# Optimization experiments

Measured on AMD Instinct MI355X. Metric: run time of the kernel, lower is better.

Reference implementation:

```python
import jax, jax.numpy as jnp
import numpy as np

H = 64
IN = 4
B = 256
T = 2048

def _uniform(key, shape, k):
    return jax.random.uniform(key, shape, jnp.float32, -k, k)

def setup_inputs() -> dict:
    key = jax.random.key(0)
    ks = jax.random.split(key, 12)
    k = 1.0 / np.sqrt(H)
    x = jax.random.normal(ks[0], (B, T, IN), jnp.float32)
    # bidirectional layer 1 (forward + backward directions); biases fused (b_ih + b_hh)
    Wih_f = _uniform(ks[1], (4 * H, IN), k); Whh_f = _uniform(ks[2], (4 * H, H), k); b_f = _uniform(ks[3], (4 * H,), k)
    Wih_b = _uniform(ks[4], (4 * H, IN), k); Whh_b = _uniform(ks[5], (4 * H, H), k); b_b = _uniform(ks[6], (4 * H,), k)
    # unidirectional layer 2, input 2H
    Wih2 = _uniform(ks[7], (4 * H, 2 * H), k); Whh2 = _uniform(ks[8], (4 * H, H), k); b2 = _uniform(ks[9], (4 * H,), k)
    Wfc = _uniform(ks[10], (1, H), k); bfc = _uniform(ks[11], (1,), k)
    return {"x": x, "Wih_f": Wih_f, "Whh_f": Whh_f, "b_f": b_f,
            "Wih_b": Wih_b, "Whh_b": Whh_b, "b_b": b_b,
            "Wih2": Wih2, "Whh2": Whh2, "b2": b2, "Wfc": Wfc, "bfc": bfc}

def _run_lstm(x, Wih, Whh, b, reverse=False):
    # x: [B, T, D] -> outputs [B, T, H], final h [B, H]
    bsz = x.shape[0]
    hdim = Whh.shape[1]
    pre = jnp.einsum('btd,gd->btg', x, Wih) + b  # [B, T, 4H], input contribution precomputed
    pre = jnp.swapaxes(pre, 0, 1)                # [T, B, 4H]
    h0 = jnp.zeros((bsz, hdim), x.dtype)
    c0 = jnp.zeros((bsz, hdim), x.dtype)
    def step(carry, p):
        h, c = carry
        g = p + h @ Whh.T
        i, f, gg, o = jnp.split(g, 4, axis=-1)  # torch gate order: i, f, g, o
        i = jax.nn.sigmoid(i); f = jax.nn.sigmoid(f)
        gg = jnp.tanh(gg); o = jax.nn.sigmoid(o)
        c = f * c + i * gg
        h = o * jnp.tanh(c)
        return (h, c), h
    (hn, _), hs = jax.lax.scan(step, (h0, c0), pre, reverse=reverse)
    return jnp.swapaxes(hs, 0, 1), hn  # [B, T, H], [B, H]

def reference(x, Wih_f, Whh_f, b_f, Wih_b, Whh_b, b_b, Wih2, Whh2, b2, Wfc, bfc):
    out_f, _ = _run_lstm(x, Wih_f, Whh_f, b_f, reverse=False)
    out_b, _ = _run_lstm(x, Wih_b, Whh_b, b_b, reverse=True)
    out1 = jnp.concatenate([out_f, out_b], axis=-1)  # [B, T, 2H]
    _, hn2 = _run_lstm(out1, Wih2, Whh2, b2, reverse=False)  # final hidden [B, H]
    logits = hn2 @ Wfc.T + bfc  # [B, 1]
    return logits
```

## Files before the change

kernel.cpp:

```cpp
#include <hip/hip_runtime.h>

#define HDIM 64
#define BATCH 256
#define TLEN 2048
#define CH 16

typedef float v2f __attribute__((ext_vector_type(2)));

__device__ __forceinline__ float rcp_fast(float x) { return __builtin_amdgcn_rcpf(x); }
__device__ __forceinline__ float sigmoid_fast(float x) { return rcp_fast(1.0f + __expf(-x)); }
__device__ __forceinline__ float tanh_fast(float x)    { return 1.0f - 2.0f * rcp_fast(1.0f + __expf(2.0f * x)); }

__device__ __forceinline__ float dpp_xor1_add(float x) {
    int v = __builtin_amdgcn_update_dpp(0, __float_as_int(x), 0xB1, 0xF, 0xF, true);
    return x + __int_as_float(v);
}
__device__ __forceinline__ float dpp_xor2_add(float x) {
    int v = __builtin_amdgcn_update_dpp(0, __float_as_int(x), 0x4E, 0xF, 0xF, true);
    return x + __int_as_float(v);
}
__device__ __forceinline__ float swz_xor4_add(float x) {
    int v = __builtin_amdgcn_ds_swizzle(__float_as_int(x), 0x101F);
    return x + __int_as_float(v);
}

__device__ __forceinline__ void pk2(v2f& acc, float ax, float ay, float bx, float by) {
    v2f a = {ax, ay}, b = {bx, by};
    acc = __builtin_elementwise_fma(a, b, acc);
}
__device__ __forceinline__ void pk4(v2f& acc, const float4 a, const float4 b) {
    pk2(acc, a.x, a.y, b.x, b.y);
    pk2(acc, a.z, a.w, b.z, b.w);
}

__global__ __launch_bounds__(256, 2)
void lstm_layer1(const float* __restrict__ x,
                 const float* __restrict__ Wih_f, const float* __restrict__ Whh_f, const float* __restrict__ b_f,
                 const float* __restrict__ Wih_b, const float* __restrict__ Whh_b, const float* __restrict__ b_b,
                 float* __restrict__ out1)
{
    const int bidx = blockIdx.x >> 1;
    const int dir  = blockIdx.x & 1;
    const float* __restrict__ Wih = dir ? Wih_b : Wih_f;
    const float* __restrict__ Whh = dir ? Whh_b : Whh_f;
    const float* __restrict__ bb  = dir ? b_b   : b_f;

    const int tid = threadIdx.x;
    const int u   = tid >> 2;
    const int p   = tid & 3;

    __shared__ float xlds[TLEN * 4];
    __shared__ float hbuf[2][HDIM];

    {
        const float4* src = (const float4*)(x + (size_t)bidx * TLEN * 4);
        float4* dst = (float4*)xlds;
        #pragma unroll
        for (int i = 0; i < 8; ++i) dst[tid + 256 * i] = src[tid + 256 * i];
    }
    if (tid < 2 * HDIM) ((float*)hbuf)[tid] = 0.f;

    const float* wbase = Whh + (size_t)u * HDIM + 16 * p;
    const float4 W00 = *(const float4*)(wbase + 0*4096 +  0), W01 = *(const float4*)(wbase + 0*4096 +  4),
                 W02 = *(const float4*)(wbase + 0*4096 +  8), W03 = *(const float4*)(wbase + 0*4096 + 12);
    const float4 W10 = *(const float4*)(wbase + 1*4096 +  0), W11 = *(const float4*)(wbase + 1*4096 +  4),
                 W12 = *(const float4*)(wbase + 1*4096 +  8), W13 = *(const float4*)(wbase + 1*4096 + 12);
    const float4 W20 = *(const float4*)(wbase + 2*4096 +  0), W21 = *(const float4*)(wbase + 2*4096 +  4),
                 W22 = *(const float4*)(wbase + 2*4096 +  8), W23 = *(const float4*)(wbase + 2*4096 + 12);
    const float4 W30 = *(const float4*)(wbase + 3*4096 +  0), W31 = *(const float4*)(wbase + 3*4096 +  4),
                 W32 = *(const float4*)(wbase + 3*4096 +  8), W33 = *(const float4*)(wbase + 3*4096 + 12);
    const float4 I0 = *(const float4*)(Wih + (0*64 + u) * 4);
    const float4 I1 = *(const float4*)(Wih + (1*64 + u) * 4);
    const float4 I2 = *(const float4*)(Wih + (2*64 + u) * 4);
    const float4 I3 = *(const float4*)(Wih + (3*64 + u) * 4);
    const float b0 = bb[u], b1 = bb[64 + u], b2g = bb[128 + u], b3 = bb[192 + u];
    __syncthreads();

    float c = 0.f;
    const float* xp = xlds + (dir ? (TLEN - 1) * 4 : 0);
    const int xstep = dir ? -4 : 4;
    float* outp = out1 + (size_t)bidx * TLEN * (2 * HDIM)
                + (size_t)(dir ? (TLEN - 1) : 0) * (2 * HDIM) + dir * HDIM + u;
    const ptrdiff_t ostep = dir ? -(2 * HDIM) : (2 * HDIM);

    #pragma unroll 2
    for (int s = 0; s < TLEN; ++s) {
        const float* hb = hbuf[s & 1];
        const float4 h0 = *(const float4*)(hb + 16 * p + 0);
        const float4 h1 = *(const float4*)(hb + 16 * p + 4);
        const float4 h2 = *(const float4*)(hb + 16 * p + 8);
        const float4 h3 = *(const float4*)(hb + 16 * p + 12);

        v2f a0 = {0.f, 0.f}, a1 = {0.f, 0.f}, a2 = {0.f, 0.f}, a3 = {0.f, 0.f};
        pk4(a0, W00, h0); pk4(a0, W01, h1); pk4(a0, W02, h2); pk4(a0, W03, h3);
        pk4(a1, W10, h0); pk4(a1, W11, h1); pk4(a1, W12, h2); pk4(a1, W13, h3);
        pk4(a2, W20, h0); pk4(a2, W21, h1); pk4(a2, W22, h2); pk4(a2, W23, h3);
        pk4(a3, W30, h0); pk4(a3, W31, h1); pk4(a3, W32, h2); pk4(a3, W33, h3);
        float g0 = a0.x + a0.y, g1 = a1.x + a1.y, g2 = a2.x + a2.y, g3 = a3.x + a3.y;

        g0 = dpp_xor2_add(dpp_xor1_add(g0));
        g1 = dpp_xor2_add(dpp_xor1_add(g1));
        g2 = dpp_xor2_add(dpp_xor1_add(g2));
        g3 = dpp_xor2_add(dpp_xor1_add(g3));

        const float4 xv = *(const float4*)xp;
        v2f e0 = {g0 + b0, 0.f}, e1 = {g1 + b1, 0.f}, e2 = {g2 + b2g, 0.f}, e3 = {g3 + b3, 0.f};
        pk4(e0, I0, xv); pk4(e1, I1, xv); pk4(e2, I2, xv); pk4(e3, I3, xv);
        g0 = e0.x + e0.y; g1 = e1.x + e1.y; g2 = e2.x + e2.y; g3 = e3.x + e3.y;

        const float ig = sigmoid_fast(g0);
        const float fg = sigmoid_fast(g1);
        const float gg = tanh_fast(g2);
        const float og = sigmoid_fast(g3);
        c = fmaf(fg, c, ig * gg);
        const float h = og * tanh_fast(c);

        if (p == 0) {
            hbuf[(s & 1) ^ 1][u] = h;
            *outp = h;
        }
        outp += ostep;
        xp   += xstep;
        __syncthreads();
    }
}

__global__ __launch_bounds__(512, 2)
void lstm_layer2(const float* __restrict__ out1,
                 const float* __restrict__ Wih2, const float* __restrict__ Whh2, const float* __restrict__ bias2,
                 const float* __restrict__ Wfc, const float* __restrict__ bfc,
                 float* __restrict__ out)
{
    const int bidx = blockIdx.x;
    const int tid  = threadIdx.x;
    const int w    = tid >> 6;
    const int lane = tid & 63;
    const int ul   = lane >> 3;
    const int p8   = lane & 7;
    const int u    = w * 8 + ul;
    const int rot  = p8 >> 1;

    __shared__ float inbuf[2][CH][2 * HDIM];
    __shared__ float hbuf[2][HDIM];

    const float* whbase = Whh2 + (size_t)u * HDIM + 8 * p8;
    const float4 H00 = *(const float4*)(whbase + 0*4096 + 0), H01 = *(const float4*)(whbase + 0*4096 + 4);
    const float4 H10 = *(const float4*)(whbase + 1*4096 + 0), H11 = *(const float4*)(whbase + 1*4096 + 4);
    const float4 H20 = *(const float4*)(whbase + 2*4096 + 0), H21 = *(const float4*)(whbase + 2*4096 + 4);
    const float4 H30 = *(const float4*)(whbase + 3*4096 + 0), H31 = *(const float4*)(whbase + 3*4096 + 4);
    const float* wibase = Wih2 + (size_t)u * 128 + 16 * p8;
    #define LWI(g, j) *(const float4*)(wibase + (g)*8192 + ((((j) + rot) & 3) << 2))
    const float4 X00 = LWI(0,0), X01 = LWI(0,1), X02 = LWI(0,2), X03 = LWI(0,3);
    const float4 X10 = LWI(1,0), X11 = LWI(1,1), X12 = LWI(1,2), X13 = LWI(1,3);
    const float4 X20 = LWI(2,0), X21 = LWI(2,1), X22 = LWI(2,2), X23 = LWI(2,3);
    const float4 X30 = LWI(3,0), X31 = LWI(3,1), X32 = LWI(3,2), X33 = LWI(3,3);
    #undef LWI
    const float b0 = bias2[u], b1 = bias2[64 + u], b2g = bias2[128 + u], b3 = bias2[192 + u];

    if (tid < 2 * HDIM) ((float*)hbuf)[tid] = 0.f;

    const float4* src = (const float4*)(out1 + (size_t)bidx * TLEN * (2 * HDIM));
    ((float4*)&inbuf[0][0][0])[tid] = src[tid];
    __syncthreads();

    float c = 0.f;

    for (int chunk = 0; chunk < TLEN / CH; ++chunk) {
        const int cb = chunk & 1;
        const bool havenext = (chunk + 1 < TLEN / CH);
        float4 pf;
        if (havenext) pf = src[(size_t)(chunk + 1) * 512 + tid];

        #pragma unroll 2
        for (int ts = 0; ts < CH; ++ts) {
            const int s = chunk * CH + ts;
            const float* hb = hbuf[s & 1];
            const float* xr = &inbuf[cb][ts][16 * p8];

            const float4 x0 = *(const float4*)(xr + (((0 + rot) & 3) << 2));
            const float4 x1 = *(const float4*)(xr + (((1 + rot) & 3) << 2));
            const float4 x2 = *(const float4*)(xr + (((2 + rot) & 3) << 2));
            const float4 x3 = *(const float4*)(xr + (((3 + rot) & 3) << 2));
            const float4 h0 = *(const float4*)(hb + 8 * p8 + 0);
            const float4 h1 = *(const float4*)(hb + 8 * p8 + 4);

            v2f a0 = {0.f, 0.f}, a1 = {0.f, 0.f}, a2 = {0.f, 0.f}, a3 = {0.f, 0.f};
            pk4(a0, X00, x0); pk4(a0, X01, x1); pk4(a0, X02, x2); pk4(a0, X03, x3);
            pk4(a0, H00, h0); pk4(a0, H01, h1);
            pk4(a1, X10, x0); pk4(a1, X11, x1); pk4(a1, X12, x2); pk4(a1, X13, x3);
            pk4(a1, H10, h0); pk4(a1, H11, h1);
            pk4(a2, X20, x0); pk4(a2, X21, x1); pk4(a2, X22, x2); pk4(a2, X23, x3);
            pk4(a2, H20, h0); pk4(a2, H21, h1);
            pk4(a3, X30, x0); pk4(a3, X31, x1); pk4(a3, X32, x2); pk4(a3, X33, x3);
            pk4(a3, H30, h0); pk4(a3, H31, h1);
            float g0 = a0.x + a0.y, g1 = a1.x + a1.y, g2 = a2.x + a2.y, g3 = a3.x + a3.y;

            g0 = swz_xor4_add(dpp_xor2_add(dpp_xor1_add(g0))) + b0;
            g1 = swz_xor4_add(dpp_xor2_add(dpp_xor1_add(g1))) + b1;
            g2 = swz_xor4_add(dpp_xor2_add(dpp_xor1_add(g2))) + b2g;
            g3 = swz_xor4_add(dpp_xor2_add(dpp_xor1_add(g3))) + b3;

            const float ig = sigmoid_fast(g0);
            const float fg = sigmoid_fast(g1);
            const float gg = tanh_fast(g2);
            const float og = sigmoid_fast(g3);
            c = fmaf(fg, c, ig * gg);
            const float h = og * tanh_fast(c);

            if (p8 == 0) hbuf[(s & 1) ^ 1][u] = h;
            __syncthreads();
        }
        if (havenext) {
            ((float4*)&inbuf[cb ^ 1][0][0])[tid] = pf;
            __syncthreads();
        }
    }

    if (w == 0) {
        float part = hbuf[0][lane] * Wfc[lane];
        #pragma unroll
        for (int m = 1; m < 64; m <<= 1) part += __shfl_xor(part, m, 64);
        if (lane == 0) out[bidx] = part + bfc[0];
    }
}

extern "C" void kernel_launch(void* const* d_in, const int* in_sizes, int n_in,
                              void* d_out, int out_size, void* d_ws, size_t ws_size,
                              hipStream_t stream) {
    const float* x     = (const float*)d_in[0];
    const float* Wih_f = (const float*)d_in[1];
    const float* Whh_f = (const float*)d_in[2];
    const float* b_f   = (const float*)d_in[3];
    const float* Wih_b = (const float*)d_in[4];
    const float* Whh_b = (const float*)d_in[5];
    const float* b_b   = (const float*)d_in[6];
    const float* Wih2  = (const float*)d_in[7];
    const float* Whh2  = (const float*)d_in[8];
    const float* b2    = (const float*)d_in[9];
    const float* Wfc   = (const float*)d_in[10];
    const float* bfc   = (const float*)d_in[11];

    float* out1 = (float*)d_ws;

    lstm_layer1<<<dim3(2 * BATCH), dim3(256), 0, stream>>>(
        x, Wih_f, Whh_f, b_f, Wih_b, Whh_b, b_b, out1);
    lstm_layer2<<<dim3(BATCH), dim3(512), 0, stream>>>(
        out1, Wih2, Whh2, b2, Wfc, bfc, (float*)d_out);
}
```

Baseline: 2.191 ms.

## Hoist layer-2 input projection into a separate parallel GEMM kernel

Adds a pre_gemm kernel that computes the layer-2 input projection (Wih2·out1 + bias) for all timesteps in parallel and writes it to workspace. The recurrent layer-2 kernel then only does the Whh2 matvec per step, using 256 threads with 4 lanes per unit instead of 512 threads. Layer 1 now batches its global output stores every 8 steps, and empty asm register pins keep weights in VGPRs. The cost is an extra 512 MB workspace write and read. If the workspace is too small, the code falls back to the old layer-2 kernel.

```diff
diff --git a/kernel.cpp b/kernel.cpp
--- a/kernel.cpp
+++ b/kernel.cpp
@@ -4,6 +4,7 @@
 #define BATCH 256
 #define TLEN 2048
 #define CH 16
+#define GTS 32
 
 typedef float v2f __attribute__((ext_vector_type(2)));
 
@@ -32,6 +33,9 @@
     pk2(acc, a.x, a.y, b.x, b.y);
     pk2(acc, a.z, a.w, b.z, b.w);
 }
+
+#define PF4(v) asm("" : "+v"((v).x), "+v"((v).y), "+v"((v).z), "+v"((v).w))
+#define PF1(v) asm("" : "+v"(v))
 
 __global__ __launch_bounds__(256, 2)
 void lstm_layer1(const float* __restrict__ x,
@@ -61,75 +65,217 @@
     if (tid < 2 * HDIM) ((float*)hbuf)[tid] = 0.f;
 
     const float* wbase = Whh + (size_t)u * HDIM + 16 * p;
-    const float4 W00 = *(const float4*)(wbase + 0*4096 +  0), W01 = *(const float4*)(wbase + 0*4096 +  4),
-                 W02 = *(const float4*)(wbase + 0*4096 +  8), W03 = *(const float4*)(wbase + 0*4096 + 12);
-    const float4 W10 = *(const float4*)(wbase + 1*4096 +  0), W11 = *(const float4*)(wbase + 1*4096 +  4),
-                 W12 = *(const float4*)(wbase + 1*4096 +  8), W13 = *(const float4*)(wbase + 1*4096 + 12);
-    const float4 W20 = *(const float4*)(wbase + 2*4096 +  0), W21 = *(const float4*)(wbase + 2*4096 +  4),
-                 W22 = *(const float4*)(wbase + 2*4096 +  8), W23 = *(const float4*)(wbase + 2*4096 + 12);
-    const float4 W30 = *(const float4*)(wbase + 3*4096 +  0), W31 = *(const float4*)(wbase + 3*4096 +  4),
-                 W32 = *(const float4*)(wbase + 3*4096 +  8), W33 = *(const float4*)(wbase + 3*4096 + 12);
-    const float4 I0 = *(const float4*)(Wih + (0*64 + u) * 4);
-    const float4 I1 = *(const float4*)(Wih + (1*64 + u) * 4);
-    const float4 I2 = *(const float4*)(Wih + (2*64 + u) * 4);
-    const float4 I3 = *(const float4*)(Wih + (3*64 + u) * 4);
-    const float b0 = bb[u], b1 = bb[64 + u], b2g = bb[128 + u], b3 = bb[192 + u];
+    float4 W00 = *(const float4*)(wbase + 0*4096 +  0), W01 = *(const float4*)(wbase + 0*4096 +  4),
+           W02 = *(const float4*)(wbase + 0*4096 +  8), W03 = *(const float4*)(wbase + 0*4096 + 12);
+    float4 W10 = *(const float4*)(wbase + 1*4096 +  0), W11 = *(const float4*)(wbase + 1*4096 +  4),
+           W12 = *(const float4*)(wbase + 1*4096 +  8), W13 = *(const float4*)(wbase + 1*4096 + 12);
+    float4 W20 = *(const float4*)(wbase + 2*4096 +  0), W21 = *(const float4*)(wbase + 2*4096 +  4),
+           W22 = *(const float4*)(wbase + 2*4096 +  8), W23 = *(const float4*)(wbase + 2*4096 + 12);
+    float4 W30 = *(const float4*)(wbase + 3*4096 +  0), W31 = *(const float4*)(wbase + 3*4096 +  4),
+           W32 = *(const float4*)(wbase + 3*4096 +  8), W33 = *(const float4*)(wbase + 3*4096 + 12);
+    float4 I0 = *(const float4*)(Wih + (0*64 + u) * 4);
+    float4 I1 = *(const float4*)(Wih + (1*64 + u) * 4);
+    float4 I2 = *(const float4*)(Wih + (2*64 + u) * 4);
+    float4 I3 = *(const float4*)(Wih + (3*64 + u) * 4);
+    float b0 = bb[u], b1 = bb[64 + u], b2g = bb[128 + u], b3 = bb[192 + u];
     __syncthreads();
 
     float c = 0.f;
     const float* xp = xlds + (dir ? (TLEN - 1) * 4 : 0);
     const int xstep = dir ? -4 : 4;
-    float* outp = out1 + (size_t)bidx * TLEN * (2 * HDIM)
-                + (size_t)(dir ? (TLEN - 1) : 0) * (2 * HDIM) + dir * HDIM + u;
+    float* ob = out1 + (size_t)bidx * TLEN * (2 * HDIM)
+              + (size_t)(dir ? (TLEN - 1) : 0) * (2 * HDIM) + dir * HDIM + u;
     const ptrdiff_t ostep = dir ? -(2 * HDIM) : (2 * HDIM);
 
-    #pragma unroll 2
-    for (int s = 0; s < TLEN; ++s) {
-        const float* hb = hbuf[s & 1];
-        const float4 h0 = *(const float4*)(hb + 16 * p + 0);
-        const float4 h1 = *(const float4*)(hb + 16 * p + 4);
-        const float4 h2 = *(const float4*)(hb + 16 * p + 8);
-        const float4 h3 = *(const float4*)(hb + 16 * p + 12);
-
-        v2f a0 = {0.f, 0.f}, a1 = {0.f, 0.f}, a2 = {0.f, 0.f}, a3 = {0.f, 0.f};
-        pk4(a0, W00, h0); pk4(a0, W01, h1); pk4(a0, W02, h2); pk4(a0, W03, h3);
-        pk4(a1, W10, h0); pk4(a1, W11, h1); pk4(a1, W12, h2); pk4(a1, W13, h3);
-        pk4(a2, W20, h0); pk4(a2, W21, h1); pk4(a2, W22, h2); pk4(a2, W23, h3);
-        pk4(a3, W30, h0); pk4(a3, W31, h1); pk4(a3, W32, h2); pk4(a3, W33, h3);
-        float g0 = a0.x + a0.y, g1 = a1.x + a1.y, g2 = a2.x + a2.y, g3 = a3.x + a3.y;
-
-        g0 = dpp_xor2_add(dpp_xor1_add(g0));
-        g1 = dpp_xor2_add(dpp_xor1_add(g1));
-        g2 = dpp_xor2_add(dpp_xor1_add(g2));
-        g3 = dpp_xor2_add(dpp_xor1_add(g3));
-
-        const float4 xv = *(const float4*)xp;
-        v2f e0 = {g0 + b0, 0.f}, e1 = {g1 + b1, 0.f}, e2 = {g2 + b2g, 0.f}, e3 = {g3 + b3, 0.f};
-        pk4(e0, I0, xv); pk4(e1, I1, xv); pk4(e2, I2, xv); pk4(e3, I3, xv);
-        g0 = e0.x + e0.y; g1 = e1.x + e1.y; g2 = e2.x + e2.y; g3 = e3.x + e3.y;
-
-        const float ig = sigmoid_fast(g0);
-        const float fg = sigmoid_fast(g1);
-        const float gg = tanh_fast(g2);
-        const float og = sigmoid_fast(g3);
-        c = fmaf(fg, c, ig * gg);
-        const float h = og * tanh_fast(c);
-
+    for (int so = 0; so < TLEN; so += 8) {
+        float hh[8];
+        #pragma unroll
+        for (int si = 0; si < 8; ++si) {
+            PF4(W00); PF4(W01); PF4(W02); PF4(W03);
+            PF4(W10); PF4(W11); PF4(W12); PF4(W13);
+            PF4(W20); PF4(W21); PF4(W22); PF4(W23);
+            PF4(W30); PF4(W31); PF4(W32); PF4(W33);
+            PF4(I0); PF4(I1); PF4(I2); PF4(I3);
+            PF1(b0); PF1(b1); PF1(b2g); PF1(b3);
+
+            const float* hb = hbuf[si & 1];
+            const float4 h0 = *(const float4*)(hb + 16 * p + 0);
+            const float4 h1 = *(const float4*)(hb + 16 * p + 4);
+            const float4 h2 = *(const float4*)(hb + 16 * p + 8);
+            const float4 h3 = *(const float4*)(hb + 16 * p + 12);
+
+            v2f a0 = {0.f, 0.f}, a1 = {0.f, 0.f}, a2 = {0.f, 0.f}, a3 = {0.f, 0.f};
+            pk4(a0, W00, h0); pk4(a0, W01, h1); pk4(a0, W02, h2); pk4(a0, W03, h3);
+            pk4(a1, W10, h0); pk4(a1, W11, h1); pk4(a1, W12, h2); pk4(a1, W13, h3);
+            pk4(a2, W20, h0); pk4(a2, W21, h1); pk4(a2, W22, h2); pk4(a2, W23, h3);
+            pk4(a3, W30, h0); pk4(a3, W31, h1); pk4(a3, W32, h2); pk4(a3, W33, h3);
+            float g0 = a0.x + a0.y, g1 = a1.x + a1.y, g2 = a2.x + a2.y, g3 = a3.x + a3.y;
+
+            g0 = dpp_xor2_add(dpp_xor1_add(g0));
+            g1 = dpp_xor2_add(dpp_xor1_add(g1));
+            g2 = dpp_xor2_add(dpp_xor1_add(g2));
+            g3 = dpp_xor2_add(dpp_xor1_add(g3));
+
+            const float4 xv = *(const float4*)(xp + si * xstep);
+            v2f e0 = {g0 + b0, 0.f}, e1 = {g1 + b1, 0.f}, e2 = {g2 + b2g, 0.f}, e3 = {g3 + b3, 0.f};
+            pk4(e0, I0, xv); pk4(e1, I1, xv); pk4(e2, I2, xv); pk4(e3, I3, xv);
+            g0 = e0.x + e0.y; g1 = e1.x + e1.y; g2 = e2.x + e2.y; g3 = e3.x + e3.y;
+
+            const float ig = sigmoid_fast(g0);
+            const float fg = sigmoid_fast(g1);
+            const float gg = tanh_fast(g2);
+            const float og = sigmoid_fast(g3);
+            c = fmaf(fg, c, ig * gg);
+            const float h = og * tanh_fast(c);
+
+            if (p == 0) hbuf[(si & 1) ^ 1][u] = h;
+            hh[si] = h;
+            __syncthreads();
+        }
         if (p == 0) {
-            hbuf[(s & 1) ^ 1][u] = h;
-            *outp = h;
-        }
-        outp += ostep;
-        xp   += xstep;
-        __syncthreads();
-    }
-}
-
-__global__ __launch_bounds__(512, 2)
-void lstm_layer2(const float* __restrict__ out1,
-                 const float* __restrict__ Wih2, const float* __restrict__ Whh2, const float* __restrict__ bias2,
+            #pragma unroll
+            for (int j = 0; j < 8; ++j) ob[j * ostep] = hh[j];
+        }
+        ob += 8 * ostep;
+        xp += 8 * xstep;
+    }
+}
+
+__global__ __launch_bounds__(256, 2)
+void pre_gemm(const float* __restrict__ out1, const float* __restrict__ Wih2,
+              const float* __restrict__ b2, float* __restrict__ pre)
+{
+    const int b  = blockIdx.x >> 6;
+    const int tc = blockIdx.x & 63;
+    const int t0 = tc * GTS;
+    const int r  = threadIdx.x;
+
+    __shared__ float xin[GTS][2 * HDIM];
+
+    const float4* s4 = (const float4*)(out1 + ((size_t)b * TLEN + t0) * (2 * HDIM));
+    #pragma unroll
+    for (int i = 0; i < 4; ++i) ((float4*)xin)[r + 256 * i] = s4[r + 256 * i];
+
+    float4 wr[32];
+    const float4* w4 = (const float4*)(Wih2 + (size_t)r * (2 * HDIM));
+    #pragma unroll
+    for (int i = 0; i < 32; ++i) wr[i] = w4[i];
+    const float bias = b2[r];
+    __syncthreads();
+
+    float* dst = pre + ((size_t)b * TLEN + t0) * 256 + r;
+    for (int t = 0; t < GTS; ++t) {
+        #pragma unroll
+        for (int i = 0; i < 32; ++i) PF4(wr[i]);
+        v2f acc = {0.f, 0.f};
+        const float4* xv = (const float4*)xin[t];
+        #pragma unroll
+        for (int i = 0; i < 32; ++i) pk4(acc, wr[i], xv[i]);
+        dst[(size_t)t * 256] = bias + acc.x + acc.y;
+    }
+}
+
+__global__ __launch_bounds__(256, 1)
+void lstm_layer2(const float* __restrict__ pre, const float* __restrict__ Whh2,
                  const float* __restrict__ Wfc, const float* __restrict__ bfc,
                  float* __restrict__ out)
+{
+    const int bidx = blockIdx.x;
+    const int tid  = threadIdx.x;
+    const int u    = tid >> 2;
+    const int p    = tid & 3;
+
+    __shared__ float prebuf[2][CH][256];
+    __shared__ float hbuf[2][HDIM];
+
+    const float* wbase = Whh2 + (size_t)u * HDIM + 16 * p;
+    float4 H00 = *(const float4*)(wbase + 0*4096 +  0), H01 = *(const float4*)(wbase + 0*4096 +  4),
+           H02 = *(const float4*)(wbase + 0*4096 +  8), H03 = *(const float4*)(wbase + 0*4096 + 12);
+    float4 H10 = *(const float4*)(wbase + 1*4096 +  0), H11 = *(const float4*)(wbase + 1*4096 +  4),
+           H12 = *(const float4*)(wbase + 1*4096 +  8), H13 = *(const float4*)(wbase + 1*4096 + 12);
+    float4 H20 = *(const float4*)(wbase + 2*4096 +  0), H21 = *(const float4*)(wbase + 2*4096 +  4),
+           H22 = *(const float4*)(wbase + 2*4096 +  8), H23 = *(const float4*)(wbase + 2*4096 + 12);
+    float4 H30 = *(const float4*)(wbase + 3*4096 +  0), H31 = *(const float4*)(wbase + 3*4096 +  4),
+           H32 = *(const float4*)(wbase + 3*4096 +  8), H33 = *(const float4*)(wbase + 3*4096 + 12);
+
+    if (tid < 2 * HDIM) ((float*)hbuf)[tid] = 0.f;
+
+    const float4* src = (const float4*)(pre + (size_t)bidx * TLEN * 256);
+    #pragma unroll
+    for (int i = 0; i < 4; ++i) ((float4*)&prebuf[0][0][0])[tid + 256 * i] = src[tid + 256 * i];
+    __syncthreads();
+
+    float c = 0.f;
+
+    for (int chunk = 0; chunk < TLEN / CH; ++chunk) {
+        const int cb = chunk & 1;
+        const bool havenext = (chunk + 1 < TLEN / CH);
+        float4 pf0, pf1, pf2, pf3;
+        if (havenext) {
+            const float4* s2 = src + (size_t)(chunk + 1) * (CH * 64);
+            pf0 = s2[tid]; pf1 = s2[tid + 256]; pf2 = s2[tid + 512]; pf3 = s2[tid + 768];
+        }
+        #pragma unroll 2
+        for (int ts = 0; ts < CH; ++ts) {
+            PF4(H00); PF4(H01); PF4(H02); PF4(H03);
+            PF4(H10); PF4(H11); PF4(H12); PF4(H13);
+            PF4(H20); PF4(H21); PF4(H22); PF4(H23);
+            PF4(H30); PF4(H31); PF4(H32); PF4(H33);
+
+            const float* hb = hbuf[ts & 1];
+            const float4 h0 = *(const float4*)(hb + 16 * p + 0);
+            const float4 h1 = *(const float4*)(hb + 16 * p + 4);
+            const float4 h2 = *(const float4*)(hb + 16 * p + 8);
+            const float4 h3 = *(const float4*)(hb + 16 * p + 12);
+
+            const float* pr = &prebuf[cb][ts][0];
+            const float q0 = pr[0 * 64 + u];
+            const float q1 = pr[1 * 64 + u];
+            const float q2 = pr[2 * 64 + u];
+            const float q3 = pr[3 * 64 + u];
+
+            v2f a0 = {0.f, 0.f}, a1 = {0.f, 0.f}, a2 = {0.f, 0.f}, a3 = {0.f, 0.f};
+            pk4(a0, H00, h0); pk4(a0, H01, h1); pk4(a0, H02, h2); pk4(a0, H03, h3);
+            pk4(a1, H10, h0); pk4(a1, H11, h1); pk4(a1, H12, h2); pk4(a1, H13, h3);
+            pk4(a2, H20, h0); pk4(a2, H21, h1); pk4(a2, H22, h2); pk4(a2, H23, h3);
+            pk4(a3, H30, h0); pk4(a3, H31, h1); pk4(a3, H32, h2); pk4(a3, H33, h3);
+            float g0 = a0.x + a0.y, g1 = a1.x + a1.y, g2 = a2.x + a2.y, g3 = a3.x + a3.y;
+
+            g0 = dpp_xor2_add(dpp_xor1_add(g0)) + q0;
+            g1 = dpp_xor2_add(dpp_xor1_add(g1)) + q1;
+            g2 = dpp_xor2_add(dpp_xor1_add(g2)) + q2;
+            g3 = dpp_xor2_add(dpp_xor1_add(g3)) + q3;
+
+            const float ig = sigmoid_fast(g0);
+            const float fg = sigmoid_fast(g1);
+            const float gg = tanh_fast(g2);
+            const float og = sigmoid_fast(g3);
+            c = fmaf(fg, c, ig * gg);
+            const float h = og * tanh_fast(c);
+
+            if (p == 0) hbuf[(ts & 1) ^ 1][u] = h;
+            __syncthreads();
+        }
+        if (havenext) {
+            float4* d4 = (float4*)&prebuf[cb ^ 1][0][0];
+            d4[tid] = pf0; d4[tid + 256] = pf1; d4[tid + 512] = pf2; d4[tid + 768] = pf3;
+            __syncthreads();
+        }
+    }
+
+    if (tid < 64) {
+        float part = hbuf[0][tid] * Wfc[tid];
+        #pragma unroll
+        for (int m = 1; m < 64; m <<= 1) part += __shfl_xor(part, m, 64);
+        if (tid == 0) out[bidx] = part + bfc[0];
+    }
+}
+
+__global__ __launch_bounds__(512, 2)
+void lstm_layer2_fb(const float* __restrict__ out1,
+                    const float* __restrict__ Wih2, const float* __restrict__ Whh2, const float* __restrict__ bias2,
+                    const float* __restrict__ Wfc, const float* __restrict__ bfc,
+                    float* __restrict__ out)
 {
     const int bidx = blockIdx.x;
     const int tid  = threadIdx.x;
@@ -173,8 +319,7 @@
 
         #pragma unroll 2
         for (int ts = 0; ts < CH; ++ts) {
-            const int s = chunk * CH + ts;
-            const float* hb = hbuf[s & 1];
+            const float* hb = hbuf[(chunk * CH + ts) & 1];
             const float* xr = &inbuf[cb][ts][16 * p8];
 
             const float4 x0 = *(const float4*)(xr + (((0 + rot) & 3) << 2));
@@ -184,7 +329,7 @@
             const float4 h0 = *(const float4*)(hb + 8 * p8 + 0);
             const float4 h1 = *(const float4*)(hb + 8 * p8 + 4);
 
-            v2f a0 = {0.f, 0.f}, a1 = {0.f, 0.f}, a2 = {0.f, 0.f}, a3 = {0.f, 0.f};
+            v2f a0 = {0.f,0.f}, a1 = {0.f,0.f}, a2 = {0.f,0.f}, a3 = {0.f,0.f};
             pk4(a0, X00, x0); pk4(a0, X01, x1); pk4(a0, X02, x2); pk4(a0, X03, x3);
             pk4(a0, H00, h0); pk4(a0, H01, h1);
             pk4(a1, X10, x0); pk4(a1, X11, x1); pk4(a1, X12, x2); pk4(a1, X13, x3);
@@ -207,7 +352,7 @@
             c = fmaf(fg, c, ig * gg);
             const float h = og * tanh_fast(c);
 
-            if (p8 == 0) hbuf[(s & 1) ^ 1][u] = h;
+            if (p8 == 0) hbuf[((chunk * CH + ts) & 1) ^ 1][u] = h;
             __syncthreads();
         }
         if (havenext) {
@@ -240,10 +385,21 @@
     const float* Wfc   = (const float*)d_in[10];
     const float* bfc   = (const float*)d_in[11];
 
+    const size_t out1_bytes = (size_t)BATCH * TLEN * 128 * 4;
+    const size_t pre_bytes  = (size_t)BATCH * TLEN * 256 * 4;
     float* out1 = (float*)d_ws;
 
     lstm_layer1<<<dim3(2 * BATCH), dim3(256), 0, stream>>>(
         x, Wih_f, Whh_f, b_f, Wih_b, Whh_b, b_b, out1);
-    lstm_layer2<<<dim3(BATCH), dim3(512), 0, stream>>>(
-        out1, Wih2, Whh2, b2, Wfc, bfc, (float*)d_out);
-}
+
+    if (ws_size >= out1_bytes + pre_bytes) {
+        float* pre = (float*)((char*)d_ws + out1_bytes);
+        pre_gemm<<<dim3(BATCH * (TLEN / GTS)), dim3(256), 0, stream>>>(
+            out1, Wih2, b2, pre);
+        lstm_layer2<<<dim3(BATCH), dim3(256), 0, stream>>>(
+            pre, Whh2, Wfc, bfc, (float*)d_out);
+    } else {
+        lstm_layer2_fb<<<dim3(BATCH), dim3(512), 0, stream>>>(
+            out1, Wih2, Whh2, b2, Wfc, bfc, (float*)d_out);
+    }
+}
```

Measured after the change: 2.317 ms. 5.7% more time.
